# Kernel tuning notes

Hardware: AMD Instinct MI355X
Metric: run time of the kernel (lower is better)

The kernel has to match this reference:

```python
import jax, jax.numpy as jnp
import numpy as np

L1_WEIGHT = 0.5
SSIM_WEIGHT = 0.5
WINDOW_SIZE = 11
SIGMA = 1.5
C1 = 0.01 ** 2
C2 = 0.03 ** 2


def _gaussian_window(dtype):
    coords = jnp.arange(WINDOW_SIZE, dtype=dtype) - (WINDOW_SIZE // 2)
    g = jnp.exp(-(coords ** 2) / (2.0 * SIGMA ** 2))
    g = g / g.sum()
    return g[:, None] * g[None, :]  # (K, K)


def _depthwise_blur(x, win2d):
    # x: (B, C, H, W); depthwise conv with shared Gaussian kernel, SAME padding
    C = x.shape[1]
    kernel = jnp.broadcast_to(win2d[None, None], (C, 1, WINDOW_SIZE, WINDOW_SIZE))
    pad = WINDOW_SIZE // 2
    return jax.lax.conv_general_dilated(
        x, kernel,
        window_strides=(1, 1),
        padding=((pad, pad), (pad, pad)),
        dimension_numbers=("NCHW", "OIHW", "NCHW"),
        feature_group_count=C,
    )


def _ssim(img1, img2):
    win = _gaussian_window(img1.dtype)
    mu1 = _depthwise_blur(img1, win)
    mu2 = _depthwise_blur(img2, win)
    mu1_sq = mu1 * mu1
    mu2_sq = mu2 * mu2
    mu1_mu2 = mu1 * mu2
    sigma1_sq = _depthwise_blur(img1 * img1, win) - mu1_sq
    sigma2_sq = _depthwise_blur(img2 * img2, win) - mu2_sq
    sigma12 = _depthwise_blur(img1 * img2, win) - mu1_mu2
    ssim_map = ((2.0 * mu1_mu2 + C1) * (2.0 * sigma12 + C2)) / (
        (mu1_sq + mu2_sq + C1) * (sigma1_sq + sigma2_sq + C2)
    )
    return ssim_map.mean()


def setup_inputs() -> dict:
    key = jax.random.key(0)
    k1, k2 = jax.random.split(key)
    shape = (32, 3, 512, 512)
    warped = jax.random.uniform(k1, shape, dtype=jnp.float32)
    target = jax.random.uniform(k2, shape, dtype=jnp.float32)
    return {"warped": warped, "target": target}


def reference(warped, target):
    l1_loss = jnp.mean(jnp.abs(warped - target))
    ssim_val = _ssim(warped, target)
    ssim_loss = 1.0 - ssim_val
    total_loss = L1_WEIGHT * l1_loss + SSIM_WEIGHT * ssim_loss
    return total_loss
```

## Files before the change

kernel.cpp:

```cpp
#include <hip/hip_runtime.h>
#include <math.h>

#define IMW 512
#define IMH 512
#define NPIX (IMW * IMH)
#define NBX 8
#define NBY 8
#define NBLK (NBX * NBY * 96)
#define C1F 1.0e-4f
#define C2F 9.0e-4f
#define PITCH 336
#define BANDB 5376
#define YOFF3 16128
#define H2BW 8064
#define H2P2 20

typedef short s16x8 __attribute__((ext_vector_type(8)));
typedef float f32x4 __attribute__((ext_vector_type(4)));
typedef float f32x2 __attribute__((ext_vector_type(2)));

__device__ __forceinline__ unsigned cvtpk(float a, float b) {
    unsigned r;
    asm("v_cvt_pk_bf16_f32 %0, %1, %2" : "=v"(r) : "v"(a), "v"(b));
    return r;
}
__device__ __forceinline__ unsigned bf16_rne(float f) {
    unsigned u = __builtin_bit_cast(unsigned, f);
    return (u + 0x7FFFu + ((u >> 16) & 1u)) >> 16;
}
__device__ __forceinline__ float bf16_to_f(unsigned b) {
    return __builtin_bit_cast(float, b << 16);
}
__device__ __forceinline__ void gload16(const void* g, void* l) {
    __builtin_amdgcn_global_load_lds(
        (const __attribute__((address_space(1))) void*)g,
        (__attribute__((address_space(3))) void*)l,
        16, 0, 0);
}
__device__ __forceinline__ f32x4 spl4(float v) { f32x4 r = {v, v, v, v}; return r; }
__device__ __forceinline__ f32x2 spl2(float v) { f32x2 r; r[0] = v; r[1] = v; return r; }
__device__ __forceinline__ f32x2 lo2(f32x4 v) { f32x2 r; r[0] = v[0]; r[1] = v[1]; return r; }
__device__ __forceinline__ f32x2 hi2(f32x4 v) { f32x2 r; r[0] = v[2]; r[1] = v[3]; return r; }

__device__ __forceinline__ f32x2 pk_mul(f32x2 a, f32x2 b) {
    f32x2 d; asm("v_pk_mul_f32 %0, %1, %2" : "=v"(d) : "v"(a), "v"(b)); return d;
}
__device__ __forceinline__ f32x2 pk_add(f32x2 a, f32x2 b) {
    f32x2 d; asm("v_pk_add_f32 %0, %1, %2" : "=v"(d) : "v"(a), "v"(b)); return d;
}
__device__ __forceinline__ f32x2 pk_sub(f32x2 a, f32x2 b) {
    f32x2 d; asm("v_pk_add_f32 %0, %1, %2 neg_lo:[0,1] neg_hi:[0,1]" : "=v"(d) : "v"(a), "v"(b)); return d;
}
__device__ __forceinline__ f32x2 pk_fma(f32x2 a, f32x2 b, f32x2 c) {
    f32x2 d; asm("v_pk_fma_f32 %0, %1, %2, %3" : "=v"(d) : "v"(a), "v"(b), "v"(c)); return d;
}
__device__ __forceinline__ f32x2 abs2(f32x2 a) {
    f32x2 d; d[0] = fabsf(a[0]); d[1] = fabsf(a[1]); return d;
}

__global__ void setup_kernel(uint4* __restrict__ wtab)
{
    const int lane = threadIdx.x;
    const int lane15 = lane & 15;
    const int g = lane >> 4;
    float w[11];
    float s = 0.f;
    for (int i = 0; i < 11; ++i) {
        const float c = (float)(i - 5);
        w[i] = expf(-(c * c) / 4.5f);
        s += w[i];
    }
    for (int i = 0; i < 11; ++i) w[i] /= s;

    s16x8 bwh, bwl, avh, avl;
    #pragma unroll
    for (int e = 0; e < 8; ++e) {
        const int k = 8 * g + e;
        const int th = k - lane15 - 3;
        const float wh = (th >= 0 && th <= 10) ? w[th] : 0.f;
        const int tv = k - lane15;
        const float wvv = (tv >= 0 && tv <= 10) ? w[tv] : 0.f;
        const unsigned h1 = bf16_rne(wh);
        const unsigned l1 = bf16_rne(wh - bf16_to_f(h1));
        bwh[e] = (short)h1; bwl[e] = (short)l1;
        const unsigned h2 = bf16_rne(wvv);
        const unsigned l2 = bf16_rne(wvv - bf16_to_f(h2));
        avh[e] = (short)h2; avl[e] = (short)l2;
    }
    wtab[lane * 4 + 0] = __builtin_bit_cast(uint4, bwh);
    wtab[lane * 4 + 1] = __builtin_bit_cast(uint4, bwl);
    wtab[lane * 4 + 2] = __builtin_bit_cast(uint4, avh);
    wtab[lane * 4 + 3] = __builtin_bit_cast(uint4, avl);
}

__global__ __launch_bounds__(256)
void ssim_l1_kernel(const float* __restrict__ warped,
                    const float* __restrict__ target,
                    const uint4* __restrict__ wtab,
                    float2* __restrict__ partial)
{
    __shared__ unsigned int LDSU[13192];

    const int tid = threadIdx.x;
    const int lane = tid & 63;
    const int wv = tid >> 6;
    const int lane15 = lane & 15;
    const int g = (lane >> 4) & 3;
    const int c0 = blockIdx.x * 64;
    const int r0 = blockIdx.y * 64;
    const size_t base = (size_t)blockIdx.z * NPIX;
    char* LB = (char*)LDSU;

    const char* xrow = (const char*)(warped + base);
    const char* yrow = (const char*)(target + base);
    const int cb0 = (c0 - 8) * 4;

    const s16x8 BwH = __builtin_bit_cast(s16x8, wtab[lane * 4 + 0]);
    const s16x8 BwL = __builtin_bit_cast(s16x8, wtab[lane * 4 + 1]);
    const s16x8 AvH = __builtin_bit_cast(s16x8, wtab[lane * 4 + 2]);
    const s16x8 AvL = __builtin_bit_cast(s16x8, wtab[lane * 4 + 3]);

    const unsigned row0 = ((unsigned)tid * 3121u) >> 16;
    const unsigned gl0  = (unsigned)tid - 21u * row0;
    const int scolb0 = min(max(cb0 + (int)(gl0 << 4), 0), 2032);
    const int ldso0 = tid * 16;
    const bool act1 = (tid < 80);
    const unsigned idx1 = (unsigned)tid + 256u;
    const unsigned row1 = (idx1 * 3121u) >> 16;
    const unsigned gl1  = idx1 - 21u * row1;
    const int scolb1 = min(max(cb0 + (int)(gl1 << 4), 0), 2032);
    const int ldso1 = (int)idx1 * 16;

    auto STAGE = [&](int t, int b) {
        const int rbase = r0 - 5 + 16 * t;
        {
            const int sr = min(max(rbase + (int)row0, 0), IMH - 1);
            const size_t rb = (size_t)sr * (IMW * 4);
            gload16(xrow + rb + scolb0, LB + b * BANDB + ldso0);
            gload16(yrow + rb + scolb0, LB + YOFF3 + b * BANDB + ldso0);
        }
        if (act1) {
            const int sr = min(max(rbase + (int)row1, 0), IMH - 1);
            const size_t rb = (size_t)sr * (IMW * 4);
            gload16(xrow + rb + scolb1, LB + b * BANDB + ldso1);
            gload16(yrow + rb + scolb1, LB + YOFF3 + b * BANDB + ldso1);
        }
    };

    const int s0 = 16 * wv + 8 * g;
    f32x4 cw0, cw1, mx0, mx1;
    #pragma unroll
    for (int e = 0; e < 4; ++e) {
        const int sA = s0 + e, sB = sA + 4;
        cw0[e] = (sA < 8 || sA > 71) ? 0.f : ((sA < 16 || sA >= 64) ? 1.f : 0.5f);
        cw1[e] = (sB < 8 || sB > 71) ? 0.f : ((sB < 16 || sB >= 64) ? 1.f : 0.5f);
        const int cA = c0 - 8 + sA, cB = c0 - 8 + sB;
        mx0[e] = ((unsigned)cA < (unsigned)IMW) ? 1.f : 0.f;
        mx1[e] = ((unsigned)cB < (unsigned)IMW) ? 1.f : 0.f;
    }
    const f32x2 cw0lo = lo2(cw0), cw0hi = hi2(cw0);
    const f32x2 cw1lo = lo2(cw1), cw1hi = hi2(cw1);
    const bool edge = (blockIdx.x == 0) || (blockIdx.x == NBX - 1) ||
                      (blockIdx.y == 0) || (blockIdx.y == NBY - 1);

    f32x2 l1a = spl2(0.f), l1b = spl2(0.f);
    f32x2 ssa = spl2(0.f), ssb = spl2(0.f);
    const f32x2 two2 = spl2(2.f), c12 = spl2(C1F), c22 = spl2(C2F);

    const int uoffE = 4 * g;
    const int uoffO = 8 - 8 * (g >> 1) + 4 * (g & 1);

    auto VPASS = [&](int ot) {
        const int uoff = (ot & 1) ? uoffO : uoffE;
        f32x4 V[4];
        __builtin_amdgcn_s_setprio(1);
        #pragma unroll
        for (int q = 0; q < 4; ++q) {
            const uint4 br = *(const uint4*)&LDSU[H2BW + ((wv * 4 + q) * 16 + lane15) * H2P2 + uoff];
            const s16x8 B = __builtin_bit_cast(s16x8, br);
            f32x4 acc = spl4(0.f);
            acc = __builtin_amdgcn_mfma_f32_16x16x32_bf16(AvH, B, acc, 0, 0, 0);
            acc = __builtin_amdgcn_mfma_f32_16x16x32_bf16(AvL, B, acc, 0, 0, 0);
            V[q] = acc;
        }
        __builtin_amdgcn_s_setprio(0);
        #pragma unroll
        for (int h = 0; h < 2; ++h) {
            const f32x2 v0 = h ? hi2(V[0]) : lo2(V[0]);
            const f32x2 v1 = h ? hi2(V[1]) : lo2(V[1]);
            const f32x2 v2 = h ? hi2(V[2]) : lo2(V[2]);
            const f32x2 v3 = h ? hi2(V[3]) : lo2(V[3]);
            const f32x2 mu12  = pk_mul(v0, v1);
            const f32x2 mu1sq = pk_mul(v0, v0);
            const f32x2 mu2sq = pk_mul(v1, v1);
            const f32x2 s12   = pk_sub(v3, mu12);
            const f32x2 ssg   = pk_sub(pk_sub(v2, mu1sq), mu2sq);
            const f32x2 num = pk_mul(pk_fma(two2, mu12, c12), pk_fma(two2, s12, c22));
            const f32x2 den = pk_mul(pk_add(pk_add(mu1sq, mu2sq), c12), pk_add(ssg, c22));
            f32x2 r;
            r[0] = __builtin_amdgcn_rcpf(den[0]);
            r[1] = __builtin_amdgcn_rcpf(den[1]);
            if (h) ssb = pk_fma(num, r, ssb);
            else   ssa = pk_fma(num, r, ssa);
        }
    };

    STAGE(0, 0);
    STAGE(1, 1);
    __builtin_amdgcn_sched_barrier(0);

    const unsigned wb = (unsigned)(s0 * 4);
    #pragma unroll
    for (int t = 0; t < 5; ++t) {
        if (t < 4) {
            if (wv < 2) asm volatile("s_waitcnt vmcnt(4)" ::: "memory");
            else        asm volatile("s_waitcnt vmcnt(2)" ::: "memory");
        } else {
            asm volatile("s_waitcnt vmcnt(0)" ::: "memory");
        }
        __builtin_amdgcn_s_barrier();
        __builtin_amdgcn_sched_barrier(0);
        if (t < 3) {
            STAGE(t + 2, (t + 2) % 3);
            __builtin_amdgcn_sched_barrier(0);
        }

        const int rs = 16 * t + lane15;
        const char* p = LB + (t % 3) * BANDB + lane15 * PITCH + wb;
        f32x4 x0 = *(const f32x4*)p;
        f32x4 x1 = *(const f32x4*)(p + 16);
        f32x4 y0 = *(const f32x4*)(p + YOFF3);
        f32x4 y1 = *(const f32x4*)(p + YOFF3 + 16);
        if (edge) {
            const float rr = ((unsigned)(r0 - 5 + rs) < (unsigned)IMH) ? 1.f : 0.f;
            const f32x4 m0 = mx0 * spl4(rr);
            const f32x4 m1 = mx1 * spl4(rr);
            x0 *= m0; x1 *= m1; y0 *= m0; y1 *= m1;
        }

        {
            const float rmL1 = (t == 0) ? ((lane15 >= 5) ? 1.f : 0.f)
                             : (t == 4) ? ((lane15 <= 4) ? 1.f : 0.f)
                             : 1.f;
            const f32x2 rm2 = spl2(rmL1);
            const f32x2 t0 = abs2(pk_sub(lo2(x0), lo2(y0)));
            const f32x2 t1 = abs2(pk_sub(hi2(x0), hi2(y0)));
            const f32x2 t2 = abs2(pk_sub(lo2(x1), lo2(y1)));
            const f32x2 t3 = abs2(pk_sub(hi2(x1), hi2(y1)));
            const f32x2 s01 = pk_fma(cw0lo, t0, pk_mul(cw1lo, t2));
            const f32x2 s23 = pk_fma(cw0hi, t1, pk_mul(cw1hi, t3));
            l1a = pk_fma(s01, rm2, l1a);
            l1b = pk_fma(s23, rm2, l1b);
        }

        const f32x2 q2al = pk_fma(lo2(x0), lo2(x0), pk_mul(lo2(y0), lo2(y0)));
        const f32x2 q2ah = pk_fma(hi2(x0), hi2(x0), pk_mul(hi2(y0), hi2(y0)));
        const f32x2 q2bl = pk_fma(lo2(x1), lo2(x1), pk_mul(lo2(y1), lo2(y1)));
        const f32x2 q2bh = pk_fma(hi2(x1), hi2(x1), pk_mul(hi2(y1), hi2(y1)));
        const f32x2 q3al = pk_mul(lo2(x0), lo2(y0));
        const f32x2 q3ah = pk_mul(hi2(x0), hi2(y0));
        const f32x2 q3bl = pk_mul(lo2(x1), lo2(y1));
        const f32x2 q3bh = pk_mul(hi2(x1), hi2(y1));

        uint4 A0u, A1u, A2u, A3u;
        A0u.x = cvtpk(x0[0], x0[1]); A0u.y = cvtpk(x0[2], x0[3]);
        A0u.z = cvtpk(x1[0], x1[1]); A0u.w = cvtpk(x1[2], x1[3]);
        A1u.x = cvtpk(y0[0], y0[1]); A1u.y = cvtpk(y0[2], y0[3]);
        A1u.z = cvtpk(y1[0], y1[1]); A1u.w = cvtpk(y1[2], y1[3]);
        A2u.x = cvtpk(q2al[0], q2al[1]); A2u.y = cvtpk(q2ah[0], q2ah[1]);
        A2u.z = cvtpk(q2bl[0], q2bl[1]); A2u.w = cvtpk(q2bh[0], q2bh[1]);
        A3u.x = cvtpk(q3al[0], q3al[1]); A3u.y = cvtpk(q3ah[0], q3ah[1]);
        A3u.z = cvtpk(q3bl[0], q3bl[1]); A3u.w = cvtpk(q3bh[0], q3bh[1]);

        const s16x8 A0 = __builtin_bit_cast(s16x8, A0u);
        const s16x8 A1 = __builtin_bit_cast(s16x8, A1u);
        const s16x8 A2 = __builtin_bit_cast(s16x8, A2u);
        const s16x8 A3 = __builtin_bit_cast(s16x8, A3u);

        f32x4 C0 = spl4(0.f), C1 = spl4(0.f), C2 = spl4(0.f), C3 = spl4(0.f);
        __builtin_amdgcn_s_setprio(1);
        C0 = __builtin_amdgcn_mfma_f32_16x16x32_bf16(A0, BwH, C0, 0, 0, 0);
        C0 = __builtin_amdgcn_mfma_f32_16x16x32_bf16(A0, BwL, C0, 0, 0, 0);
        C1 = __builtin_amdgcn_mfma_f32_16x16x32_bf16(A1, BwH, C1, 0, 0, 0);
        C1 = __builtin_amdgcn_mfma_f32_16x16x32_bf16(A1, BwL, C1, 0, 0, 0);
        C2 = __builtin_amdgcn_mfma_f32_16x16x32_bf16(A2, BwH, C2, 0, 0, 0);
        C2 = __builtin_amdgcn_mfma_f32_16x16x32_bf16(A2, BwL, C2, 0, 0, 0);
        C3 = __builtin_amdgcn_mfma_f32_16x16x32_bf16(A3, BwH, C3, 0, 0, 0);
        C3 = __builtin_amdgcn_mfma_f32_16x16x32_bf16(A3, BwL, C3, 0, 0, 0);
        __builtin_amdgcn_s_setprio(0);

        #pragma unroll
        for (int q = 0; q < 4; ++q) {
            const f32x4 Cq = (q == 0) ? C0 : (q == 1) ? C1 : (q == 2) ? C2 : C3;
            uint2 pp;
            pp.x = cvtpk(Cq[0], Cq[1]);
            pp.y = cvtpk(Cq[2], Cq[3]);
            *(uint2*)&LDSU[H2BW + ((wv * 4 + q) * 16 + lane15) * H2P2 + (t & 1) * 8 + 2 * g] = pp;
        }

        if (t >= 1) VPASS(t - 1);
    }

    float l1sum = (l1a[0] + l1a[1]) + (l1b[0] + l1b[1]);
    float ssum  = (ssa[0] + ssa[1]) + (ssb[0] + ssb[1]);
    #pragma unroll
    for (int off = 32; off > 0; off >>= 1) {
        l1sum += __shfl_down(l1sum, off);
        ssum  += __shfl_down(ssum,  off);
    }
    float* red = (float*)&LDSU[13184];
    if (lane == 0) { red[wv] = l1sum; red[4 + wv] = ssum; }
    __syncthreads();
    if (tid == 0) {
        const float L1 = red[0] + red[1] + red[2] + red[3];
        const float SS = red[4] + red[5] + red[6] + red[7];
        const int bid = (blockIdx.z * gridDim.y + blockIdx.y) * gridDim.x + blockIdx.x;
        partial[bid] = make_float2(L1, SS);
    }
}

__global__ __launch_bounds__(256)
void reduce_kernel(const float2* __restrict__ partial, float* __restrict__ out)
{
    double l1 = 0.0, ss = 0.0;
    for (int i = threadIdx.x; i < NBLK; i += 256) {
        const float2 p = partial[i];
        l1 += (double)p.x;
        ss += (double)p.y;
    }
    #pragma unroll
    for (int off = 32; off > 0; off >>= 1) {
        l1 += __shfl_down(l1, off);
        ss += __shfl_down(ss, off);
    }
    __shared__ double red[8];
    const int wv = threadIdx.x >> 6, lane = threadIdx.x & 63;
    if (lane == 0) { red[wv] = l1; red[4 + wv] = ss; }
    __syncthreads();
    if (threadIdx.x == 0) {
        const double n = 25165824.0;
        const double L1 = (red[0] + red[1] + red[2] + red[3]) / n;
        const double SS = (red[4] + red[5] + red[6] + red[7]) / n;
        out[0] = (float)(0.5 * L1 + 0.5 * (1.0 - SS));
    }
}

extern "C" void kernel_launch(void* const* d_in, const int* in_sizes, int n_in,
                              void* d_out, int out_size, void* d_ws, size_t ws_size,
                              hipStream_t stream)
{
    const float* warped = (const float*)d_in[0];
    const float* target = (const float*)d_in[1];
    float* out = (float*)d_out;
    uint4* wtab = (uint4*)d_ws;
    float2* partial = (float2*)((char*)d_ws + 4096);

    hipLaunchKernelGGL(setup_kernel, dim3(1), dim3(64), 0, stream, wtab);
    hipLaunchKernelGGL(ssim_l1_kernel, dim3(NBX, NBY, 96), dim3(256), 0, stream,
                       warped, target, wtab, partial);
    hipLaunchKernelGGL(reduce_kernel, dim3(1), dim3(256), 0, stream, partial, out);
}
```

Baseline: 78.38 us.

## Load input bands directly to registers instead of staging through LDS

Replaces the global_load_lds triple-buffered staging of input row bands with per-thread direct global loads into a double-buffered register set, prefetching two bands ahead. This removes the LDS staging traffic, the barriers and waitcnt sync per band, and shrinks LDS from about 52KB to about 20KB, which may allow more resident blocks. The cost is more VGPRs for prefetch buffers, less coalesced per-thread 32-byte loads, and edge masking now also triggered when the column clamp shifts.

Measured after the change: 80.58 us. +2.8%, slower.

```diff
diff --git a/kernel.cpp b/kernel.cpp
--- a/kernel.cpp
+++ b/kernel.cpp
@@ -9,10 +9,6 @@
 #define NBLK (NBX * NBY * 96)
 #define C1F 1.0e-4f
 #define C2F 9.0e-4f
-#define PITCH 336
-#define BANDB 5376
-#define YOFF3 16128
-#define H2BW 8064
 #define H2P2 20
 
 typedef short s16x8 __attribute__((ext_vector_type(8)));
@@ -30,12 +26,6 @@
 }
 __device__ __forceinline__ float bf16_to_f(unsigned b) {
     return __builtin_bit_cast(float, b << 16);
-}
-__device__ __forceinline__ void gload16(const void* g, void* l) {
-    __builtin_amdgcn_global_load_lds(
-        (const __attribute__((address_space(1))) void*)g,
-        (__attribute__((address_space(3))) void*)l,
-        16, 0, 0);
 }
 __device__ __forceinline__ f32x4 spl4(float v) { f32x4 r = {v, v, v, v}; return r; }
 __device__ __forceinline__ f32x2 spl2(float v) { f32x2 r; r[0] = v; r[1] = v; return r; }
@@ -99,7 +89,7 @@
                     const uint4* __restrict__ wtab,
                     float2* __restrict__ partial)
 {
-    __shared__ unsigned int LDSU[13192];
+    __shared__ unsigned int LDSU[5128];
 
     const int tid = threadIdx.x;
     const int lane = tid & 63;
@@ -109,45 +99,19 @@
     const int c0 = blockIdx.x * 64;
     const int r0 = blockIdx.y * 64;
     const size_t base = (size_t)blockIdx.z * NPIX;
-    char* LB = (char*)LDSU;
-
-    const char* xrow = (const char*)(warped + base);
-    const char* yrow = (const char*)(target + base);
-    const int cb0 = (c0 - 8) * 4;
+
+    const char* xc = (const char*)(warped + base);
+    const char* yc = (const char*)(target + base);
 
     const s16x8 BwH = __builtin_bit_cast(s16x8, wtab[lane * 4 + 0]);
     const s16x8 BwL = __builtin_bit_cast(s16x8, wtab[lane * 4 + 1]);
     const s16x8 AvH = __builtin_bit_cast(s16x8, wtab[lane * 4 + 2]);
     const s16x8 AvL = __builtin_bit_cast(s16x8, wtab[lane * 4 + 3]);
 
-    const unsigned row0 = ((unsigned)tid * 3121u) >> 16;
-    const unsigned gl0  = (unsigned)tid - 21u * row0;
-    const int scolb0 = min(max(cb0 + (int)(gl0 << 4), 0), 2032);
-    const int ldso0 = tid * 16;
-    const bool act1 = (tid < 80);
-    const unsigned idx1 = (unsigned)tid + 256u;
-    const unsigned row1 = (idx1 * 3121u) >> 16;
-    const unsigned gl1  = idx1 - 21u * row1;
-    const int scolb1 = min(max(cb0 + (int)(gl1 << 4), 0), 2032);
-    const int ldso1 = (int)idx1 * 16;
-
-    auto STAGE = [&](int t, int b) {
-        const int rbase = r0 - 5 + 16 * t;
-        {
-            const int sr = min(max(rbase + (int)row0, 0), IMH - 1);
-            const size_t rb = (size_t)sr * (IMW * 4);
-            gload16(xrow + rb + scolb0, LB + b * BANDB + ldso0);
-            gload16(yrow + rb + scolb0, LB + YOFF3 + b * BANDB + ldso0);
-        }
-        if (act1) {
-            const int sr = min(max(rbase + (int)row1, 0), IMH - 1);
-            const size_t rb = (size_t)sr * (IMW * 4);
-            gload16(xrow + rb + scolb1, LB + b * BANDB + ldso1);
-            gload16(yrow + rb + scolb1, LB + YOFF3 + b * BANDB + ldso1);
-        }
-    };
-
     const int s0 = 16 * wv + 8 * g;
+    const int cb0 = (c0 - 8) * 4;
+    const int colb = min(max(cb0 + s0 * 4, 0), 2016);
+
     f32x4 cw0, cw1, mx0, mx1;
     #pragma unroll
     for (int e = 0; e < 4; ++e) {
@@ -161,7 +125,8 @@
     const f32x2 cw0lo = lo2(cw0), cw0hi = hi2(cw0);
     const f32x2 cw1lo = lo2(cw1), cw1hi = hi2(cw1);
     const bool edge = (blockIdx.x == 0) || (blockIdx.x == NBX - 1) ||
-                      (blockIdx.y == 0) || (blockIdx.y == NBY - 1);
+                      (blockIdx.y == 0) || (blockIdx.y == NBY - 1) ||
+                      (colb != cb0 + s0 * 4);
 
     f32x2 l1a = spl2(0.f), l1b = spl2(0.f);
     f32x2 ssa = spl2(0.f), ssb = spl2(0.f);
@@ -176,7 +141,7 @@
         __builtin_amdgcn_s_setprio(1);
         #pragma unroll
         for (int q = 0; q < 4; ++q) {
-            const uint4 br = *(const uint4*)&LDSU[H2BW + ((wv * 4 + q) * 16 + lane15) * H2P2 + uoff];
+            const uint4 br = *(const uint4*)&LDSU[((wv * 4 + q) * 16 + lane15) * H2P2 + uoff];
             const s16x8 B = __builtin_bit_cast(s16x8, br);
             f32x4 acc = spl4(0.f);
             acc = __builtin_amdgcn_mfma_f32_16x16x32_bf16(AvH, B, acc, 0, 0, 0);
@@ -205,34 +170,28 @@
         }
     };
 
-    STAGE(0, 0);
-    STAGE(1, 1);
-    __builtin_amdgcn_sched_barrier(0);
-
-    const unsigned wb = (unsigned)(s0 * 4);
+    f32x4 P0[4], P1[4];
+    auto LOADB = [&](int t, f32x4* dst) {
+        const int rsl = min(max(r0 - 5 + 16 * t + lane15, 0), IMH - 1);
+        const char* px = xc + (size_t)rsl * (IMW * 4) + colb;
+        const char* py = yc + (size_t)rsl * (IMW * 4) + colb;
+        dst[0] = *(const f32x4*)px;
+        dst[1] = *(const f32x4*)(px + 16);
+        dst[2] = *(const f32x4*)py;
+        dst[3] = *(const f32x4*)(py + 16);
+    };
+
+    LOADB(0, P0);
+    LOADB(1, P1);
+
     #pragma unroll
     for (int t = 0; t < 5; ++t) {
-        if (t < 4) {
-            if (wv < 2) asm volatile("s_waitcnt vmcnt(4)" ::: "memory");
-            else        asm volatile("s_waitcnt vmcnt(2)" ::: "memory");
-        } else {
-            asm volatile("s_waitcnt vmcnt(0)" ::: "memory");
-        }
-        __builtin_amdgcn_s_barrier();
-        __builtin_amdgcn_sched_barrier(0);
-        if (t < 3) {
-            STAGE(t + 2, (t + 2) % 3);
-            __builtin_amdgcn_sched_barrier(0);
-        }
-
-        const int rs = 16 * t + lane15;
-        const char* p = LB + (t % 3) * BANDB + lane15 * PITCH + wb;
-        f32x4 x0 = *(const f32x4*)p;
-        f32x4 x1 = *(const f32x4*)(p + 16);
-        f32x4 y0 = *(const f32x4*)(p + YOFF3);
-        f32x4 y1 = *(const f32x4*)(p + YOFF3 + 16);
+        f32x4* B = (t & 1) ? P1 : P0;
+        f32x4 x0 = B[0], x1 = B[1], y0 = B[2], y1 = B[3];
+        if (t + 2 < 5) LOADB(t + 2, B);
+
         if (edge) {
-            const float rr = ((unsigned)(r0 - 5 + rs) < (unsigned)IMH) ? 1.f : 0.f;
+            const float rr = ((unsigned)(r0 - 5 + 16 * t + lane15) < (unsigned)IMH) ? 1.f : 0.f;
             const f32x4 m0 = mx0 * spl4(rr);
             const f32x4 m1 = mx1 * spl4(rr);
             x0 *= m0; x1 *= m1; y0 *= m0; y1 *= m1;
@@ -295,7 +254,7 @@
             uint2 pp;
             pp.x = cvtpk(Cq[0], Cq[1]);
             pp.y = cvtpk(Cq[2], Cq[3]);
-            *(uint2*)&LDSU[H2BW + ((wv * 4 + q) * 16 + lane15) * H2P2 + (t & 1) * 8 + 2 * g] = pp;
+            *(uint2*)&LDSU[((wv * 4 + q) * 16 + lane15) * H2P2 + (t & 1) * 8 + 2 * g] = pp;
         }
 
         if (t >= 1) VPASS(t - 1);
@@ -308,7 +267,7 @@
         l1sum += __shfl_down(l1sum, off);
         ssum  += __shfl_down(ssum,  off);
     }
-    float* red = (float*)&LDSU[13184];
+    float* red = (float*)&LDSU[5120];
     if (lane == 0) { red[wv] = l1sum; red[4 + wv] = ssum; }
     __syncthreads();
     if (tid == 0) {
```
